# Optimization experiments

Measured on AMD Instinct MI355X. Metric: run time of the kernel, lower is better.

## Reference

```python
import jax, jax.numpy as jnp
import numpy as np

OUT = 7          # roi_layer out_size
SR = 2           # roi_layer sample_num (sampling ratio)
STRIDES = (4, 8, 16, 32)
FINEST_SCALE = 56.0


def roi_align_level(feat, rois, spatial_scale):
    """RoIAlign (aligned=False, torchvision/mmdet classic) for all rois on one level.
    feat: (B, C, H, W), rois: (K, 5) [batch_idx, x1, y1, x2, y2] in image coords.
    Returns (K, C, OUT, OUT)."""
    B, C, H, W = feat.shape
    b = rois[:, 0].astype(jnp.int32)
    x1 = rois[:, 1] * spatial_scale
    y1 = rois[:, 2] * spatial_scale
    x2 = rois[:, 3] * spatial_scale
    y2 = rois[:, 4] * spatial_scale
    roi_w = jnp.maximum(x2 - x1, 1.0)
    roi_h = jnp.maximum(y2 - y1, 1.0)
    bin_w = roi_w / OUT
    bin_h = roi_h / OUT
    # per-bin sample offsets: (OUT, SR) fractional bin positions
    off = jnp.arange(OUT, dtype=jnp.float32)[:, None] + (jnp.arange(SR, dtype=jnp.float32)[None, :] + 0.5) / SR
    ys = y1[:, None, None] + off[None] * bin_h[:, None, None]   # (K, OUT, SR)
    xs = x1[:, None, None] + off[None] * bin_w[:, None, None]   # (K, OUT, SR)
    y = ys[:, :, :, None, None]                                  # (K, OUT, SR, 1, 1)
    x = xs[:, None, None, :, :]                                  # (K, 1, 1, OUT, SR)
    y, x = jnp.broadcast_arrays(y, x)                            # (K, OUT, SR, OUT, SR)
    valid = (y > -1.0) & (y < H) & (x > -1.0) & (x < W)
    yc = jnp.clip(y, 0.0, H - 1.0)
    xc = jnp.clip(x, 0.0, W - 1.0)
    y0 = jnp.floor(yc)
    x0 = jnp.floor(xc)
    ly = yc - y0
    lx = xc - x0
    hy = 1.0 - ly
    hx = 1.0 - lx
    y0i = y0.astype(jnp.int32)
    x0i = x0.astype(jnp.int32)
    y1i = jnp.minimum(y0i + 1, H - 1)
    x1i = jnp.minimum(x0i + 1, W - 1)
    bb = jnp.broadcast_to(b[:, None, None, None, None], y0i.shape)

    def g(yi, xi):
        # advanced indexing (batched gather) -> (K, OUT, SR, OUT, SR, C)
        return feat[bb, :, yi, xi]

    val = (hy * hx)[..., None] * g(y0i, x0i) \
        + (hy * lx)[..., None] * g(y0i, x1i) \
        + (ly * hx)[..., None] * g(y1i, x0i) \
        + (ly * lx)[..., None] * g(y1i, x1i)
    val = jnp.where(valid[..., None], val, 0.0)
    pooled = val.mean(axis=(2, 4))           # average SRxSR samples -> (K, OUT, OUT, C)
    return jnp.transpose(pooled, (0, 3, 1, 2))  # (K, C, OUT, OUT)


def map_roi_levels(rois, num_levels):
    scale = jnp.sqrt((rois[:, 3] - rois[:, 1] + 1.0) * (rois[:, 4] - rois[:, 2] + 1.0))
    lvl = jnp.floor(jnp.log2(scale / FINEST_SCALE + 1e-6))
    return jnp.clip(lvl, 0, num_levels - 1).astype(jnp.int32)


def setup_inputs() -> dict:
    key = jax.random.key(0)
    ks = jax.random.split(key, 10)
    B, C = 2, 256
    IMG_H, IMG_W = 800.0, 1344.0
    feats = {}
    shapes = [(B, C, 200, 336), (B, C, 100, 168), (B, C, 50, 84), (B, C, 25, 42)]
    for i, s in enumerate(shapes):
        feats[f"feat{i}"] = jax.random.normal(ks[i], s, dtype=jnp.float32)
    K = 1024
    bidx = jax.random.randint(ks[4], (K,), 0, B).astype(jnp.float32)
    # log-uniform box sizes in [16, ~724] px so all 4 FPN levels get rois
    w = 2.0 ** jax.random.uniform(ks[5], (K,), minval=4.0, maxval=9.5)
    h = 2.0 ** jax.random.uniform(ks[6], (K,), minval=4.0, maxval=9.5)
    cx = jax.random.uniform(ks[7], (K,), minval=0.0, maxval=IMG_W)
    cy = jax.random.uniform(ks[8], (K,), minval=0.0, maxval=IMG_H)
    x1 = jnp.clip(cx - w * 0.5, 0.0, IMG_W - 2.0)
    y1 = jnp.clip(cy - h * 0.5, 0.0, IMG_H - 2.0)
    x2 = jnp.clip(x1 + w, x1 + 1.0, IMG_W - 1.0)
    y2 = jnp.clip(y1 + h, y1 + 1.0, IMG_H - 1.0)
    rois = jnp.stack([bidx, x1, y1, x2, y2], axis=-1).astype(jnp.float32)
    feats["rois"] = rois
    return feats


def reference(feat0, feat1, feat2, feat3, rois):
    feats = [feat0, feat1, feat2, feat3]
    num_levels = len(feats)
    target_lvls = map_roi_levels(rois, num_levels)
    K = rois.shape[0]
    C = feats[0].shape[1]
    roi_feats = jnp.zeros((K, C, OUT, OUT), dtype=feats[0].dtype)
    for i in range(num_levels):
        ri = roi_align_level(feats[i], rois, 1.0 / STRIDES[i])
        mask = (target_lvls == i)[:, None, None, None]
        roi_feats = roi_feats + jnp.where(mask, ri, 0.0)
    return roi_feats
```

## Files before the change

kernel.cpp:

```cpp
#include <hip/hip_runtime.h>
#include <stdint.h>
#include <stddef.h>

#define C_TOTAL   256
#define CPG       8
#define NGROUPS   (C_TOTAL / CPG)
#define NBINS     49
#define NSAMP     196
#define TILE_D    1152
#define SD_STRIDE 16
#define BLOB_DW   (NSAMP * 4)
#define SORTN     1024


__global__ __launch_bounds__(256)
void roi_desc_kernel(const float* __restrict__ rois, int* __restrict__ ws_i,
                     int blobBase, int kbase)
{
    const int k   = blockIdx.x;
    const int tid = threadIdx.x;

    const float bf  = rois[k * 5 + 0];
    const float rx1 = rois[k * 5 + 1];
    const float ry1 = rois[k * 5 + 2];
    const float rx2 = rois[k * 5 + 3];
    const float ry2 = rois[k * 5 + 4];
    const int   b   = (int)bf;

    const float scale = sqrtf((rx2 - rx1 + 1.0f) * (ry2 - ry1 + 1.0f));
    int lvl = (int)floorf(log2f(scale / 56.0f + 1e-6f));
    lvl = lvl < 0 ? 0 : (lvl > 3 ? 3 : lvl);

    int H, W;
    if      (lvl == 0) { H = 200; W = 336; }
    else if (lvl == 1) { H = 100; W = 168; }
    else if (lvl == 2) { H =  50; W =  84; }
    else               { H =  25; W =  42; }

    const float ss  = 1.0f / (float)(4 << lvl);
    const float x1s = rx1 * ss, y1s = ry1 * ss;
    const float x2s = rx2 * ss, y2s = ry2 * ss;
    const float roi_w = fmaxf(x2s - x1s, 1.0f);
    const float roi_h = fmaxf(y2s - y1s, 1.0f);
    const float bw = roi_w * (1.0f / 7.0f);
    const float bh = roi_h * (1.0f / 7.0f);

    const float Hm1 = (float)(H - 1), Wm1 = (float)(W - 1);
    const int ty0 = (int)floorf(fminf(fmaxf(y1s + 0.25f * bh, 0.0f), Hm1));
    const int tx0 = (int)floorf(fminf(fmaxf(x1s + 0.25f * bw, 0.0f), Wm1));
    const int ty1 = min((int)floorf(fminf(fmaxf(y1s + 6.75f * bh, 0.0f), Hm1)) + 1, H - 1);
    const int tx1 = min((int)floorf(fminf(fmaxf(x1s + 6.75f * bw, 0.0f), Wm1)) + 1, W - 1);
    const int fh = ty1 - ty0 + 1;
    const int fw = tx1 - tx0 + 1;

    int cpr = (fw + (tx0 & 3) + 3) >> 2;
    if (cpr > (W >> 2)) cpr = W >> 2;
    const bool use16 = (lvl < 3) && (fh * cpr <= TILE_D / 4);

    int rb, rowStride, chunks;
    if (use16) {
        rb = tx0 & ~3;
        if (rb + 4 * cpr > W) rb = W - 4 * cpr;
        rowStride = 4 * cpr;
        chunks = fh * cpr;
        if (chunks > TILE_D / 4) chunks = TILE_D / 4;
    } else {
        rb = tx0;
        rowStride = fw;
        chunks = fh * fw;
        if (chunks > TILE_D) chunks = TILE_D;
    }
    const uint32_t d = use16 ? (uint32_t)cpr : (uint32_t)fw;
    const uint32_t M = (1u << 22) / d + 1u;
    const int dW = W - rowStride;

    if (tid == 0) {
        int* sd = ws_i + k * SD_STRIDE;
        sd[0] = lvl;
        sd[1] = use16 ? 1 : 0;
        sd[2] = b * C_TOTAL * H * W + ty0 * W + rb;
        sd[3] = chunks;
        sd[4] = (int)M;
        sd[5] = dW;
        sd[6] = H * W;
        sd[7] = k;
        const float cx = 0.5f * (rx1 + rx2);
        const float cy = 0.5f * (ry1 + ry2);
        int qx = (int)(cx * (64.0f / 1344.0f));
        int qy = (int)(cy * (64.0f / 800.0f));
        qx = qx < 0 ? 0 : (qx > 63 ? 63 : qx);
        qy = qy < 0 ? 0 : (qy > 63 ? 63 : qy);
        unsigned m = 0;
#pragma unroll
        for (int j = 0; j < 6; ++j)
            m |= (((unsigned)(qx >> j) & 1u) << (2 * j)) |
                 (((unsigned)(qy >> j) & 1u) << (2 * j + 1));
        ws_i[kbase + k] = (int)(((unsigned)lvl << 23) | ((unsigned)b << 22)
                                | (m << 10) | (unsigned)k);
    }

    if (tid < NSAMP) {
        const int iy = tid / 14;
        const int ix = tid - iy * 14;
        const float yy = y1s + ((float)iy * 0.5f + 0.25f) * bh;
        const float xx = x1s + ((float)ix * 0.5f + 0.25f) * bw;
        const bool valid = (yy > -1.0f) && (yy < (float)H) && (xx > -1.0f) && (xx < (float)W);
        const float yc  = fminf(fmaxf(yy, 0.0f), Hm1);
        const float xc  = fminf(fmaxf(xx, 0.0f), Wm1);
        const float y0f = floorf(yc);
        const float x0f = floorf(xc);
        const float ly = yc - y0f, lx = xc - x0f;
        const int y0  = (int)y0f, x0 = (int)x0f;
        const int y1i = min(y0 + 1, H - 1);
        const int x1i = min(x0 + 1, W - 1);
        const int r0 = (y0  - ty0) * rowStride - rb;
        const int rd = (y1i - y0) * rowStride;
        const int dx = x1i - x0;
        const int pack = (valid ? 0 : (int)0x80000000) | (rd << 1) | dx;
        int4* blob = (int4*)(ws_i + blobBase + (size_t)k * BLOB_DW);
        blob[tid] = make_int4(r0 + x0, pack,
                              __float_as_int(lx), __float_as_int(ly));
    }
}

__global__ __launch_bounds__(256)
void roi_sort_kernel(int* __restrict__ ws_i, int K, int kbase, int sbase)
{
    __shared__ unsigned skey[SORTN];
    const int tid = threadIdx.x;

    const bool do_sort = (K <= SORTN);
    if (do_sort) {
        for (int i = tid; i < SORTN; i += 256)
            skey[i] = (i < K) ? (unsigned)ws_i[kbase + i] : 0xFFFFFFFFu;
        __syncthreads();
        for (unsigned size = 2; size <= SORTN; size <<= 1) {
            for (unsigned stride = size >> 1; stride; stride >>= 1) {
                for (int i = tid; i < SORTN; i += 256) {
                    const unsigned p = (unsigned)i ^ stride;
                    if (p > (unsigned)i) {
                        const bool up = ((i & size) == 0);
                        const unsigned a = skey[i], b = skey[p];
                        if ((a > b) == up) { skey[i] = b; skey[p] = a; }
                    }
                }
                __syncthreads();
            }
        }
    }
    for (int i = tid; i < K * SD_STRIDE; i += 256) {
        const int rank = i >> 4, j = i & 15;
        const int k = do_sort ? (int)(skey[rank] & 1023u) : rank;
        ws_i[sbase + i] = ws_i[k * SD_STRIDE + j];
    }
}

__global__ __launch_bounds__(512, 8)
void roi_align_main(const float* __restrict__ f0,
                    const float* __restrict__ f1,
                    const float* __restrict__ f2,
                    const float* __restrict__ f3,
                    const int* __restrict__ ws_i,
                    float* __restrict__ out,
                    int blobBase, int sbase)
{
    __shared__ __align__(16) float s_tile[CPG * TILE_D];
    __shared__ __align__(16) float s_desc[BLOB_DW];

    const int rank = blockIdx.y;
    const int g    = blockIdx.x;
    const int tid  = threadIdx.x;
    const int wv   = tid >> 6;
    const int lane = tid & 63;

    const int* sd = ws_i + sbase + rank * SD_STRIDE;
    const int lvl     = sd[0];
    const int use16   = sd[1];
    const int srcBase = sd[2];
    const int chunks  = sd[3];
    const uint32_t M  = (uint32_t)sd[4];
    const int dW      = sd[5];
    const int HW      = sd[6];
    const int k       = sd[7];

    const float* feat = (lvl == 0) ? f0 : (lvl == 1) ? f1 : (lvl == 2) ? f2 : f3;

    if (wv < 4) {
        const int i0 = (wv < 3) ? (wv << 6) : (NSAMP - 64);
        const float* bsrc = (const float*)(ws_i + blobBase + (size_t)k * BLOB_DW);
        __builtin_amdgcn_global_load_lds(
            (const __attribute__((address_space(1))) uint32_t*)(bsrc + ((i0 + lane) << 2)),
            (__attribute__((address_space(3))) uint32_t*)(s_desc + (i0 << 2)),
            16, 0, 0);
    }

    {
        const int c = g * CPG + wv;
        const float* src = feat + srcBase + (size_t)c * (size_t)HW;
        float* dst = s_tile + wv * TILE_D;
        if (use16) {
            for (int start = 0; start < chunks; start += 64) {
                int s = (start + 64 > chunks) ? max(chunks - 64, 0) : start;
                int idx = s + lane;
                if (idx >= chunks) idx = chunks - 1;
                const int fy  = (int)(((uint32_t)idx * M) >> 22);
                const int off = (idx << 2) + fy * dW;
                __builtin_amdgcn_global_load_lds(
                    (const __attribute__((address_space(1))) uint32_t*)(src + off),
                    (__attribute__((address_space(3))) uint32_t*)(dst + (s << 2)),
                    16, 0, 0);
            }
        } else {
            for (int start = 0; start < chunks; start += 64) {
                int s = (start + 64 > chunks) ? max(chunks - 64, 0) : start;
                int idx = s + lane;
                if (idx >= chunks) idx = chunks - 1;
                const int fy  = (int)(((uint32_t)idx * M) >> 22);
                const int off = idx + fy * dW;
                __builtin_amdgcn_global_load_lds(
                    (const __attribute__((address_space(1))) uint32_t*)(src + off),
                    (__attribute__((address_space(3))) uint32_t*)(dst + s),
                    4, 0, 0);
            }
        }
    }

    asm volatile("s_waitcnt vmcnt(0)" ::: "memory");
    __syncthreads();

    if (lane < NBINS) {
        const float* t   = s_tile + wv * TILE_D;
        const int4*  dsc = (const int4*)s_desc;
        const int oy = lane / 7;
        const int ox = lane - oy * 7;
        const int sbin = oy * 28 + ox * 2;
        float acc = 0.0f;
#pragma unroll
        for (int sy = 0; sy < 2; ++sy) {
#pragma unroll
            for (int sx = 0; sx < 2; ++sx) {
                const int4 dcp = dsc[sbin + sy * 14 + sx];
                const float lx = __int_as_float(dcp.z);
                const float ly = __int_as_float(dcp.w);
                const float hx = 1.0f - lx, hy = 1.0f - ly;
                const float v  = (dcp.y < 0) ? 0.0f : 0.25f;
                const int dx  = dcp.y & 1;
                const int rd  = (dcp.y >> 1) & 0xFFFF;
                const int c00 = dcp.x;
                acc += (hy * hx * v) * t[c00]
                     + (hy * lx * v) * t[c00 + dx]
                     + (ly * hx * v) * t[c00 + rd]
                     + (ly * lx * v) * t[c00 + rd + dx];
            }
        }
        const int c = g * CPG + wv;
        out[((size_t)k * C_TOTAL + c) * NBINS + lane] = acc;
    }
}

extern "C" void kernel_launch(void* const* d_in, const int* in_sizes, int n_in,
                              void* d_out, int out_size, void* d_ws, size_t ws_size,
                              hipStream_t stream) {
    const float* f0   = (const float*)d_in[0];
    const float* f1   = (const float*)d_in[1];
    const float* f2   = (const float*)d_in[2];
    const float* f3   = (const float*)d_in[3];
    const float* rois = (const float*)d_in[4];
    float* out = (float*)d_out;
    int*   ws  = (int*)d_ws;

    const int K = in_sizes[4] / 5;
    const int blobBase = K * SD_STRIDE;
    const int kbase    = blobBase + K * BLOB_DW;
    const int sbase    = kbase + SORTN;

    roi_desc_kernel<<<K, 256, 0, stream>>>(rois, ws, blobBase, kbase);
    roi_sort_kernel<<<1, 256, 0, stream>>>(ws, K, kbase, sbase);

    dim3 grid(NGROUPS, K, 1);
    roi_align_main<<<grid, 512, 0, stream>>>(f0, f1, f2, f3, ws, out, blobBase, sbase);
}
```

Measured before the change: 135.1 us.

## Convert RoIAlign main kernel to persistent per-wave task loop

Replaces the (channel-group × roi) grid with a fixed grid of 8192 blocks where each wave independently processes (roi, channel) tasks in a strided loop. Task order is channel-major across sorted roi ranks, descriptors are read directly from global memory into registers instead of staged in LDS, and the next task's metadata is prefetched before waiting on the current tile load. This removes block-level __syncthreads and the descriptor LDS staging and lets waves proceed independently, at the cost of less descriptor reuse across waves and reliance on per-wave LDS regions without barriers.

```diff
diff --git a/kernel.cpp b/kernel.cpp
--- a/kernel.cpp
+++ b/kernel.cpp
@@ -3,14 +3,14 @@
 #include <stddef.h>
 
 #define C_TOTAL   256
-#define CPG       8
-#define NGROUPS   (C_TOTAL / CPG)
 #define NBINS     49
 #define NSAMP     196
 #define TILE_D    1152
 #define SD_STRIDE 16
 #define BLOB_DW   (NSAMP * 4)
 #define SORTN     1024
+#define NBLK      8192
+#define WPB       8
 
 
 __global__ __launch_bounds__(256)
@@ -162,84 +162,90 @@
                     const float* __restrict__ f3,
                     const int* __restrict__ ws_i,
                     float* __restrict__ out,
-                    int blobBase, int sbase)
+                    int blobBase, int sbase, int K)
 {
-    __shared__ __align__(16) float s_tile[CPG * TILE_D];
-    __shared__ __align__(16) float s_desc[BLOB_DW];
-
-    const int rank = blockIdx.y;
-    const int g    = blockIdx.x;
+    __shared__ __align__(16) float s_tile[WPB * TILE_D];
+
     const int tid  = threadIdx.x;
     const int wv   = tid >> 6;
     const int lane = tid & 63;
-
-    const int* sd = ws_i + sbase + rank * SD_STRIDE;
-    const int lvl     = sd[0];
-    const int use16   = sd[1];
-    const int srcBase = sd[2];
-    const int chunks  = sd[3];
-    const uint32_t M  = (uint32_t)sd[4];
-    const int dW      = sd[5];
-    const int HW      = sd[6];
-    const int k       = sd[7];
-
-    const float* feat = (lvl == 0) ? f0 : (lvl == 1) ? f1 : (lvl == 2) ? f2 : f3;
-
-    if (wv < 4) {
-        const int i0 = (wv < 3) ? (wv << 6) : (NSAMP - 64);
-        const float* bsrc = (const float*)(ws_i + blobBase + (size_t)k * BLOB_DW);
-        __builtin_amdgcn_global_load_lds(
-            (const __attribute__((address_space(1))) uint32_t*)(bsrc + ((i0 + lane) << 2)),
-            (__attribute__((address_space(3))) uint32_t*)(s_desc + (i0 << 2)),
-            16, 0, 0);
-    }
-
-    {
-        const int c = g * CPG + wv;
-        const float* src = feat + srcBase + (size_t)c * (size_t)HW;
-        float* dst = s_tile + wv * TILE_D;
-        if (use16) {
-            for (int start = 0; start < chunks; start += 64) {
-                int s = (start + 64 > chunks) ? max(chunks - 64, 0) : start;
-                int idx = s + lane;
-                if (idx >= chunks) idx = chunks - 1;
-                const int fy  = (int)(((uint32_t)idx * M) >> 22);
-                const int off = (idx << 2) + fy * dW;
-                __builtin_amdgcn_global_load_lds(
-                    (const __attribute__((address_space(1))) uint32_t*)(src + off),
-                    (__attribute__((address_space(3))) uint32_t*)(dst + (s << 2)),
-                    16, 0, 0);
+    const int Wid  = blockIdx.x * WPB + wv;
+    const int totalW = NBLK * WPB;
+    const int nTask  = K * C_TOTAL;
+
+    const int oy = lane / 7;
+    const int ox = lane - oy * 7;
+    const int sbin = (lane < NBINS) ? (oy * 28 + ox * 2) : 0;
+
+    float* dst = s_tile + wv * TILE_D;
+
+    int T = Wid;
+    if (T >= nTask) return;
+
+    int rank = T % K;
+    const int* sp = ws_i + sbase + rank * SD_STRIDE;
+    int lvl = sp[0], use16 = sp[1], srcBase = sp[2], chunks = sp[3];
+    uint32_t M = (uint32_t)sp[4];
+    int dW = sp[5], HW = sp[6], k = sp[7];
+
+    while (true) {
+        const int c = T / K;
+        const float* feat = (lvl == 0) ? f0 : (lvl == 1) ? f1 : (lvl == 2) ? f2 : f3;
+
+        const int4* dg = (const int4*)(ws_i + blobBase + (size_t)k * BLOB_DW);
+        const int4 d0 = dg[sbin];
+        const int4 d1 = dg[sbin + 1];
+        const int4 d2 = dg[sbin + 14];
+        const int4 d3 = dg[sbin + 15];
+
+        {
+            const float* src = feat + srcBase + (size_t)c * (size_t)HW;
+            if (use16) {
+                for (int start = 0; start < chunks; start += 64) {
+                    int s = (start + 64 > chunks) ? max(chunks - 64, 0) : start;
+                    int idx = s + lane;
+                    if (idx >= chunks) idx = chunks - 1;
+                    const int fy  = (int)(((uint32_t)idx * M) >> 22);
+                    const int off = (idx << 2) + fy * dW;
+                    __builtin_amdgcn_global_load_lds(
+                        (const __attribute__((address_space(1))) uint32_t*)(src + off),
+                        (__attribute__((address_space(3))) uint32_t*)(dst + (s << 2)),
+                        16, 0, 0);
+                }
+            } else {
+                for (int start = 0; start < chunks; start += 64) {
+                    int s = (start + 64 > chunks) ? max(chunks - 64, 0) : start;
+                    int idx = s + lane;
+                    if (idx >= chunks) idx = chunks - 1;
+                    const int fy  = (int)(((uint32_t)idx * M) >> 22);
+                    const int off = idx + fy * dW;
+                    __builtin_amdgcn_global_load_lds(
+                        (const __attribute__((address_space(1))) uint32_t*)(src + off),
+                        (__attribute__((address_space(3))) uint32_t*)(dst + s),
+                        4, 0, 0);
+                }
             }
-        } else {
-            for (int start = 0; start < chunks; start += 64) {
-                int s = (start + 64 > chunks) ? max(chunks - 64, 0) : start;
-                int idx = s + lane;
-                if (idx >= chunks) idx = chunks - 1;
-                const int fy  = (int)(((uint32_t)idx * M) >> 22);
-                const int off = idx + fy * dW;
-                __builtin_amdgcn_global_load_lds(
-                    (const __attribute__((address_space(1))) uint32_t*)(src + off),
-                    (__attribute__((address_space(3))) uint32_t*)(dst + s),
-                    4, 0, 0);
-            }
-        }
-    }
-
-    asm volatile("s_waitcnt vmcnt(0)" ::: "memory");
-    __syncthreads();
-
-    if (lane < NBINS) {
-        const float* t   = s_tile + wv * TILE_D;
-        const int4*  dsc = (const int4*)s_desc;
-        const int oy = lane / 7;
-        const int ox = lane - oy * 7;
-        const int sbin = oy * 28 + ox * 2;
-        float acc = 0.0f;
+        }
+
+        const int Tn = T + totalW;
+        const bool more = (Tn < nTask);
+        int lvl2 = 0, use162 = 0, srcBase2 = 0, chunks2 = 0, dW2 = 0, HW2 = 0, k2 = 0;
+        uint32_t M2 = 0;
+        if (more) {
+            const int r2 = Tn % K;
+            const int* sq = ws_i + sbase + r2 * SD_STRIDE;
+            lvl2 = sq[0]; use162 = sq[1]; srcBase2 = sq[2]; chunks2 = sq[3];
+            M2 = (uint32_t)sq[4]; dW2 = sq[5]; HW2 = sq[6]; k2 = sq[7];
+        }
+
+        asm volatile("s_waitcnt vmcnt(0)" ::: "memory");
+
+        if (lane < NBINS) {
+            const float* t = dst;
+            float acc = 0.0f;
 #pragma unroll
-        for (int sy = 0; sy < 2; ++sy) {
-#pragma unroll
-            for (int sx = 0; sx < 2; ++sx) {
-                const int4 dcp = dsc[sbin + sy * 14 + sx];
+            for (int j = 0; j < 4; ++j) {
+                const int4 dcp = (j == 0) ? d0 : (j == 1) ? d1 : (j == 2) ? d2 : d3;
                 const float lx = __int_as_float(dcp.z);
                 const float ly = __int_as_float(dcp.w);
                 const float hx = 1.0f - lx, hy = 1.0f - ly;
@@ -252,9 +258,13 @@
                      + (ly * hx * v) * t[c00 + rd]
                      + (ly * lx * v) * t[c00 + rd + dx];
             }
-        }
-        const int c = g * CPG + wv;
-        out[((size_t)k * C_TOTAL + c) * NBINS + lane] = acc;
+            out[((size_t)k * C_TOTAL + c) * NBINS + lane] = acc;
+        }
+
+        if (!more) break;
+        T = Tn;
+        lvl = lvl2; use16 = use162; srcBase = srcBase2; chunks = chunks2;
+        M = M2; dW = dW2; HW = HW2; k = k2;
     }
 }
 
@@ -277,6 +287,6 @@
     roi_desc_kernel<<<K, 256, 0, stream>>>(rois, ws, blobBase, kbase);
     roi_sort_kernel<<<1, 256, 0, stream>>>(ws, K, kbase, sbase);
 
-    dim3 grid(NGROUPS, K, 1);
-    roi_align_main<<<grid, 512, 0, stream>>>(f0, f1, f2, f3, ws, out, blobBase, sbase);
-}
+    roi_align_main<<<NBLK, 512, 0, stream>>>(f0, f1, f2, f3, ws, out,
+                                             blobBase, sbase, K);
+}
```

After: 179.2 us. 32.7% more time.
